# Kernel optimization log

Hardware: AMD Instinct MI355X
Metric: run time of the kernel (lower is better)

The kernel has to match this reference:

```python
import jax, jax.numpy as jnp
import numpy as np

WINDOW = 128  # crop size (compute_crops default window_size)


def centre_crop(centroids, window_size, h, w):
    # centroids: [C,2] int; returns flat gather coords [2, C*ws*ws]
    half = window_size // 2
    cy = jnp.clip(centroids[:, 0], half, h - half)
    cx = jnp.clip(centroids[:, 1], half, w - half)
    gy, gx = jnp.meshgrid(jnp.arange(window_size), jnp.arange(window_size), indexing='ij')
    rows = (cy - half)[:, None, None] + gy[None]  # [C,ws,ws]
    cols = (cx - half)[:, None, None] + gx[None]
    return jnp.stack([rows.reshape(-1), cols.reshape(-1)])  # [2, C*ws*ws]


def setup_inputs() -> dict:
    key = jax.random.key(0)
    ks = jax.random.split(key, 8)
    E, S, C, H, W = 6, 1, 512, 1024, 1024
    Dh = 16
    return {
        'x': jax.random.normal(ks[0], (E, H, W), dtype=jnp.float32),
        'sigma': jax.random.uniform(ks[1], (S, H, W), dtype=jnp.float32),
        'c': jax.random.normal(ks[2], (C, E), dtype=jnp.float32),
        'W1': jax.random.normal(ks[3], (E + S, Dh), dtype=jnp.float32) * 0.3,
        'b1': jnp.zeros((Dh,), dtype=jnp.float32),
        'W2': jax.random.normal(ks[4], (Dh, Dh), dtype=jnp.float32) * 0.3,
        'b2': jnp.zeros((Dh,), dtype=jnp.float32),
        'W3': jax.random.normal(ks[5], (Dh, 1), dtype=jnp.float32) * 0.3,
        'b3': jnp.zeros((1,), dtype=jnp.float32),
        'centroids_idx': jax.random.randint(ks[6], (C, 2), 0, H, dtype=jnp.int32),
    }


def reference(x, sigma, c, W1, b1, W2, b2, W3, b3, centroids_idx):
    E, h, w = x.shape
    S = sigma.shape[0]
    C = c.shape[0]
    ws = WINDOW
    mesh = centre_crop(centroids_idx, ws, h, w)  # [2, C*ws*ws]
    # gather per-instance windows from concatenated embedding+sigma maps
    xs = jnp.concatenate([x, sigma], axis=0)  # [E+S, H, W]
    g = xs[:, mesh[0], mesh[1]]               # [E+S, C*ws*ws]
    g = g.reshape(E + S, C, ws, ws).transpose(1, 0, 2, 3)  # [C, E+S, ws, ws]
    # subtract centroid descriptor from embedding channels (feature_engineering '0')
    g = jnp.concatenate([g[:, :E] - c[:, :, None, None], g[:, E:]], axis=1)
    feats = g.transpose(0, 2, 3, 1).reshape(-1, E + S)  # [(C*ws*ws), E+S]
    # per-pixel probability MLP (ProbabilityNet)
    hdn = jax.nn.relu(feats @ W1 + b1)
    hdn = jax.nn.relu(hdn @ W2 + b2)
    prob = jax.nn.sigmoid(hdn @ W3 + b3)
    prob = prob.reshape(C, 1, ws, ws)
    # instance-id / coordinate table for the downstream scatter (iidd)
    inst = jnp.repeat(jnp.arange(C, dtype=mesh.dtype), ws * ws)
    iidd = jnp.concatenate([inst[None], mesh], axis=0)  # [3, C*ws*ws]
    return prob, iidd
```

## Files before the change

kernel.cpp:

```cpp
#include <hip/hip_runtime.h>

#define WS 128
#define HW (1024 * 1024)
#define PLANE 8388608

typedef _Float16 half4 __attribute__((ext_vector_type(4)));
typedef _Float16 half8 __attribute__((ext_vector_type(8)));
typedef float floatx4 __attribute__((ext_vector_type(4)));

__global__ __launch_bounds__(256) void precompute_G(
    const float* __restrict__ x,
    const float* __restrict__ sigma,
    _Float16* __restrict__ G)
{
    const int px = blockIdx.x * 256 + threadIdx.x;
    half8 g;
#pragma unroll
    for (int e = 0; e < 6; ++e) g[e] = (_Float16)x[e * HW + px];
    g[6] = (_Float16)sigma[px];
    g[7] = (_Float16)0.0f;
    *(half8*)(G + (size_t)px * 8) = g;
}

__global__ __launch_bounds__(256) void instanseg_mlp(
    const _Float16* __restrict__ G,
    const float* __restrict__ c,
    const float* __restrict__ W1,
    const float* __restrict__ b1,
    const float* __restrict__ W2,
    const float* __restrict__ b2,
    const float* __restrict__ W3,
    const float* __restrict__ b3,
    const int*   __restrict__ cent,
    float* __restrict__ out)
{
    const int cid  = blockIdx.y;
    const int lane = threadIdx.x & 63;
    const int wave = threadIdx.x >> 6;
    const int quad = lane >> 4;
    const int sub  = lane & 15;

    const int cy = min(max(cent[2 * cid], 64), 960);
    const int cx = min(max(cent[2 * cid + 1], 64), 960);
    const int cy0 = cy - 64, cx0 = cx - 64;

    half4 a1;
#pragma unroll
    for (int i = 0; i < 4; ++i) {
        const int k = 4 * quad + i;
        a1[i] = (k < 7) ? (_Float16)W1[k * 16 + sub] : (_Float16)0.0f;
    }

    half4 a2;
    float w3f[4], bb2[4], qf[4];
#pragma unroll
    for (int i = 0; i < 4; ++i) {
        const int k = 4 * quad + i;
        a2[i]  = (_Float16)W2[k * 16 + sub];
        w3f[i] = W3[k];
        bb2[i] = b2[k];
        float qv = -b1[k];
#pragma unroll
        for (int e = 0; e < 6; ++e)
            qv = fmaf(W1[e * 16 + k], c[cid * 6 + e], qv);
        qf[i] = qv;
    }
    const float b3v = b3[0];
    const floatx4 zero = {0.0f, 0.0f, 0.0f, 0.0f};

    const int wavestart = blockIdx.x * 2048 + wave * 512;

    half4 v[4], vn[4];
#pragma unroll
    for (int ch = 0; ch < 4; ++ch) { v[ch] = (half4)(_Float16)0.0f; vn[ch] = (half4)(_Float16)0.0f; }
    {
        const int base = (cy0 + (wavestart >> 7)) * 1024 + cx0 + sub;
        const _Float16* rowp = G + (size_t)base * 8 + quad * 4;
        if (quad < 2) {
#pragma unroll
            for (int ch = 0; ch < 4; ++ch)
                v[ch] = *(const half4*)(rowp + ch * 128);
        }
    }

    for (int it = 0; it < 8; ++it) {
        const int start = wavestart + it * 64;

        if (it < 7) {
            const int nstart = start + 64;
            const int base = (cy0 + (nstart >> 7)) * 1024 + cx0 + (nstart & 127) + sub;
            const _Float16* rowp = G + (size_t)base * 8 + quad * 4;
            if (quad < 2) {
#pragma unroll
                for (int ch = 0; ch < 4; ++ch)
                    vn[ch] = *(const half4*)(rowp + ch * 128);
            }
        }

        float logit[4];
#pragma unroll
        for (int ch = 0; ch < 4; ++ch) {
            floatx4 c1 = __builtin_amdgcn_mfma_f32_16x16x16f16(a1, v[ch], zero, 0, 0, 0);

            half4 h;
#pragma unroll
            for (int i = 0; i < 4; ++i)
                h[i] = (_Float16)fmaxf(c1[i] - qf[i], 0.0f);

            floatx4 c2 = __builtin_amdgcn_mfma_f32_16x16x16f16(a2, h, zero, 0, 0, 0);

            float part = 0.0f;
#pragma unroll
            for (int i = 0; i < 4; ++i)
                part = fmaf(w3f[i], fmaxf(c2[i] + bb2[i], 0.0f), part);
            part += __shfl_xor(part, 16, 64);
            part += __shfl_xor(part, 32, 64);
            logit[ch] = part;
        }

        const float l01 = (quad & 1) ? logit[1] : logit[0];
        const float l23 = (quad & 1) ? logit[3] : logit[2];
        const float lg  = (quad & 2) ? l23 : l01;
        const float prob = 1.0f / (1.0f + __expf(-(lg + b3v)));

        const int rowy = cy0 + (start >> 7);
        const int colx = cx0 + (start & 127) + lane;
        const int n    = cid * 16384 + start + lane;
        out[n]             = prob;
        out[PLANE + n]     = (float)cid;
        out[2 * PLANE + n] = (float)rowy;
        out[3 * PLANE + n] = (float)colx;

        if (it < 7) {
#pragma unroll
            for (int ch = 0; ch < 4; ++ch) v[ch] = vn[ch];
        }
    }
}

extern "C" void kernel_launch(void* const* d_in, const int* in_sizes, int n_in,
                              void* d_out, int out_size, void* d_ws, size_t ws_size,
                              hipStream_t stream) {
    const float* x     = (const float*)d_in[0];
    const float* sigma = (const float*)d_in[1];
    const float* c     = (const float*)d_in[2];
    const float* W1    = (const float*)d_in[3];
    const float* b1    = (const float*)d_in[4];
    const float* W2    = (const float*)d_in[5];
    const float* b2    = (const float*)d_in[6];
    const float* W3    = (const float*)d_in[7];
    const float* b3    = (const float*)d_in[8];
    const int*   cent  = (const int*)d_in[9];
    float* out = (float*)d_out;
    _Float16* G = (_Float16*)d_ws;

    precompute_G<<<dim3(HW / 256), dim3(256), 0, stream>>>(x, sigma, G);
    instanseg_mlp<<<dim3(8, 512), dim3(256), 0, stream>>>(
        G, c, W1, b1, W2, b2, W3, b3, cent, out);
}
```

Before: 193.8 us.

## Prefetch two iterations ahead and fold biases into MFMA accumulators

The MLP kernel now keeps a three-stage register pipeline, loading input tiles two iterations ahead instead of one, to hide more global memory latency. The first- and second-layer bias terms (including the centroid offset) are passed as the MFMA accumulator input rather than being subtracted or added afterwards, which removes per-element VALU ops. The cost is extra registers for the additional prefetch buffer.

Result: slower. 199.5 us (+3.0%).

```diff
diff --git a/kernel.cpp b/kernel.cpp
--- a/kernel.cpp
+++ b/kernel.cpp
@@ -52,67 +52,77 @@
     }
 
     half4 a2;
-    float w3f[4], bb2[4], qf[4];
+    float w3f[4];
+    floatx4 cq, cb;
 #pragma unroll
     for (int i = 0; i < 4; ++i) {
         const int k = 4 * quad + i;
         a2[i]  = (_Float16)W2[k * 16 + sub];
         w3f[i] = W3[k];
-        bb2[i] = b2[k];
-        float qv = -b1[k];
+        cb[i]  = b2[k];
+        float qv = b1[k];
 #pragma unroll
         for (int e = 0; e < 6; ++e)
-            qv = fmaf(W1[e * 16 + k], c[cid * 6 + e], qv);
-        qf[i] = qv;
+            qv = fmaf(-W1[e * 16 + k], c[cid * 6 + e], qv);
+        cq[i] = qv;
     }
     const float b3v = b3[0];
-    const floatx4 zero = {0.0f, 0.0f, 0.0f, 0.0f};
 
     const int wavestart = blockIdx.x * 2048 + wave * 512;
 
-    half4 v[4], vn[4];
+    half4 v[4], vn[4], vn2[4];
 #pragma unroll
-    for (int ch = 0; ch < 4; ++ch) { v[ch] = (half4)(_Float16)0.0f; vn[ch] = (half4)(_Float16)0.0f; }
+    for (int ch = 0; ch < 4; ++ch) {
+        v[ch] = (half4)(_Float16)0.0f;
+        vn[ch] = (half4)(_Float16)0.0f;
+        vn2[ch] = (half4)(_Float16)0.0f;
+    }
     {
-        const int base = (cy0 + (wavestart >> 7)) * 1024 + cx0 + sub;
-        const _Float16* rowp = G + (size_t)base * 8 + quad * 4;
+        const int base0 = (cy0 + (wavestart >> 7)) * 1024 + cx0 + sub;
+        const _Float16* rowp0 = G + (size_t)base0 * 8 + quad * 4;
+        const int n1 = wavestart + 64;
+        const int base1 = (cy0 + (n1 >> 7)) * 1024 + cx0 + (n1 & 127) + sub;
+        const _Float16* rowp1 = G + (size_t)base1 * 8 + quad * 4;
         if (quad < 2) {
 #pragma unroll
             for (int ch = 0; ch < 4; ++ch)
-                v[ch] = *(const half4*)(rowp + ch * 128);
+                v[ch] = *(const half4*)(rowp0 + ch * 128);
+#pragma unroll
+            for (int ch = 0; ch < 4; ++ch)
+                vn[ch] = *(const half4*)(rowp1 + ch * 128);
         }
     }
 
     for (int it = 0; it < 8; ++it) {
         const int start = wavestart + it * 64;
 
-        if (it < 7) {
-            const int nstart = start + 64;
+        if (it < 6) {
+            const int nstart = start + 128;
             const int base = (cy0 + (nstart >> 7)) * 1024 + cx0 + (nstart & 127) + sub;
             const _Float16* rowp = G + (size_t)base * 8 + quad * 4;
             if (quad < 2) {
 #pragma unroll
                 for (int ch = 0; ch < 4; ++ch)
-                    vn[ch] = *(const half4*)(rowp + ch * 128);
+                    vn2[ch] = *(const half4*)(rowp + ch * 128);
             }
         }
 
         float logit[4];
 #pragma unroll
         for (int ch = 0; ch < 4; ++ch) {
-            floatx4 c1 = __builtin_amdgcn_mfma_f32_16x16x16f16(a1, v[ch], zero, 0, 0, 0);
+            floatx4 c1 = __builtin_amdgcn_mfma_f32_16x16x16f16(a1, v[ch], cq, 0, 0, 0);
 
             half4 h;
 #pragma unroll
             for (int i = 0; i < 4; ++i)
-                h[i] = (_Float16)fmaxf(c1[i] - qf[i], 0.0f);
+                h[i] = (_Float16)fmaxf(c1[i], 0.0f);
 
-            floatx4 c2 = __builtin_amdgcn_mfma_f32_16x16x16f16(a2, h, zero, 0, 0, 0);
+            floatx4 c2 = __builtin_amdgcn_mfma_f32_16x16x16f16(a2, h, cb, 0, 0, 0);
 
             float part = 0.0f;
 #pragma unroll
             for (int i = 0; i < 4; ++i)
-                part = fmaf(w3f[i], fmaxf(c2[i] + bb2[i], 0.0f), part);
+                part = fmaf(w3f[i], fmaxf(c2[i], 0.0f), part);
             part += __shfl_xor(part, 16, 64);
             part += __shfl_xor(part, 32, 64);
             logit[ch] = part;
@@ -131,10 +141,8 @@
         out[2 * PLANE + n] = (float)rowy;
         out[3 * PLANE + n] = (float)colx;
 
-        if (it < 7) {
 #pragma unroll
-            for (int ch = 0; ch < 4; ++ch) v[ch] = vn[ch];
-        }
+        for (int ch = 0; ch < 4; ++ch) { v[ch] = vn[ch]; vn[ch] = vn2[ch]; }
     }
 }
 
```
